# Kernel optimization log

Measured on AMD Instinct MI355X. Metric: run time of the kernel, lower is better.

## Reference

```python
import jax, jax.numpy as jnp
import numpy as np


def setup_inputs() -> dict:
    key = jax.random.key(0)
    ks = jax.random.split(key, 12)
    B, N, D_in, D = 64, 512, 512, 512
    inp = {
        "x": jax.random.normal(ks[0], (B, N, D_in), dtype=jnp.float32),
        "adj": jax.random.uniform(ks[1], (B, N, N), dtype=jnp.float32),
        "mask": jnp.ones((B, N, 1), dtype=jnp.float32),
        "W_enc": jax.random.normal(ks[2], (D_in, D), dtype=jnp.float32) * (1.0 / np.sqrt(D_in)),
        "b_enc": jnp.zeros((D,), dtype=jnp.float32),
        "Wz": jax.random.normal(ks[3], (D, D), dtype=jnp.float32) * (1.0 / np.sqrt(D)),
        "Uz": jax.random.normal(ks[4], (D, D), dtype=jnp.float32) * (1.0 / np.sqrt(D)),
        "bz": jnp.zeros((D,), dtype=jnp.float32),
        "Wr": jax.random.normal(ks[5], (D, D), dtype=jnp.float32) * (1.0 / np.sqrt(D)),
        "Ur": jax.random.normal(ks[6], (D, D), dtype=jnp.float32) * (1.0 / np.sqrt(D)),
        "br": jnp.zeros((D,), dtype=jnp.float32),
        "Wh": jax.random.normal(ks[7], (D, D), dtype=jnp.float32) * (1.0 / np.sqrt(D)),
        "Uh": jax.random.normal(ks[8], (D, D), dtype=jnp.float32) * (1.0 / np.sqrt(D)),
        "bh": jnp.zeros((D,), dtype=jnp.float32),
        "ba": jnp.zeros((D,), dtype=jnp.float32),
        "steps": 2,
    }
    return inp


def _gru_step(h, adj, mask, Wz, Uz, bz, Wr, Ur, br, Wh, Uh, bh, ba, act):
    # aggregated neighbor messages: [B,N,D]
    a = jnp.einsum('bnm,bmd->bnd', adj, h) + ba
    z = act(a @ Wz + h @ Uz + bz)          # update gate
    r = act(a @ Wr + h @ Ur + br)          # reset gate
    hc = jnp.tanh(a @ Wh + (r * h) @ Uh + bh)
    hc = hc * mask
    return (1.0 - z) * h + z * hc


def reference(x, adj, mask, W_enc, b_enc, Wz, Uz, bz, Wr, Ur, br, Wh, Uh, bh, ba, steps):
    act = jax.nn.relu
    h = mask * act(x @ W_enc + b_enc)      # [B,N,D]
    for _ in range(steps):
        h = _gru_step(h, adj, mask, Wz, Uz, bz, Wr, Ur, br, Wh, Uh, bh, ba, act)
    return h
```

## Files before the change

### kernel.cpp

```cpp
#include <hip/hip_runtime.h>


#define LD 512
#define CFENCE asm volatile("" ::: "memory")

typedef unsigned short u16;
typedef _Float16 f16;
typedef f16 f16x8 __attribute__((ext_vector_type(8)));
typedef float f32x4 __attribute__((ext_vector_type(4)));

__device__ __forceinline__ u16 f2h(float f) { f16 h = (f16)f; return *(u16*)&h; }
__device__ __forceinline__ float h2f(u16 b) { f16 h = *(f16*)&b; return (float)h; }

__device__ __forceinline__ void gload16(const void* g, void* l) {
  __builtin_amdgcn_global_load_lds(
      (const __attribute__((address_space(1))) void*)g,
      (__attribute__((address_space(3))) void*)l, 16, 0, 0);
}

__global__ void cvt_f16(const float* __restrict__ in, u16* __restrict__ out, int n4) {
  int i = blockIdx.x * blockDim.x + threadIdx.x;
  if (i >= n4) return;
  float4 v = reinterpret_cast<const float4*>(in)[i];
  ushort4 o;
  o.x = f2h(v.x); o.y = f2h(v.y); o.z = f2h(v.z); o.w = f2h(v.w);
  reinterpret_cast<ushort4*>(out)[i] = o;
}

__global__ void cvt2h(const float* __restrict__ in, u16* __restrict__ ohi,
                      u16* __restrict__ olo, int n4) {
  int i = blockIdx.x * blockDim.x + threadIdx.x;
  if (i >= n4) return;
  float4 v = reinterpret_cast<const float4*>(in)[i];
  ushort4 h, l;
  h.x = f2h(v.x); l.x = f2h(v.x - h2f(h.x));
  h.y = f2h(v.y); l.y = f2h(v.y - h2f(h.y));
  h.z = f2h(v.z); l.z = f2h(v.z - h2f(h.z));
  h.w = f2h(v.w); l.w = f2h(v.w - h2f(h.w));
  reinterpret_cast<ushort4*>(ohi)[i] = h;
  reinterpret_cast<ushort4*>(olo)[i] = l;
}

__global__ void wconv1(const float* __restrict__ in, u16* __restrict__ out, float scale) {
  __shared__ float sm[32][33];
  int tx = threadIdx.x & 31, ty = threadIdx.x >> 5;
  int k0 = blockIdx.y * 32, n0 = blockIdx.x * 32;
#pragma unroll
  for (int i = 0; i < 32; i += 8)
    sm[ty + i][tx] = in[(size_t)(k0 + ty + i) * LD + n0 + tx];
  __syncthreads();
#pragma unroll
  for (int i = 0; i < 32; i += 8)
    out[(size_t)(n0 + ty + i) * LD + k0 + tx] = f2h(sm[tx][ty + i] * scale);
}

__global__ void wconv2h(const float* __restrict__ in, u16* __restrict__ ohi,
                        u16* __restrict__ olo, float scale) {
  __shared__ float sm[32][33];
  int tx = threadIdx.x & 31, ty = threadIdx.x >> 5;
  int k0 = blockIdx.y * 32, n0 = blockIdx.x * 32;
#pragma unroll
  for (int i = 0; i < 32; i += 8)
    sm[ty + i][tx] = in[(size_t)(k0 + ty + i) * LD + n0 + tx];
  __syncthreads();
#pragma unroll
  for (int i = 0; i < 32; i += 8) {
    float v = sm[tx][ty + i] * scale;
    u16 hi = f2h(v);
    size_t o = (size_t)(n0 + ty + i) * LD + k0 + tx;
    ohi[o] = hi;
    olo[o] = f2h(v - h2f(hi));
  }
}

__global__ void transp16(const u16* __restrict__ in, u16* __restrict__ out) {
  __shared__ u16 sm[64][65];
  int b = blockIdx.z;
  int n0 = blockIdx.y * 64, d0 = blockIdx.x * 64;
  int lane = threadIdx.x & 63, grp = threadIdx.x >> 6;
  const u16* src = in + ((size_t)b * LD + n0) * LD + d0;
#pragma unroll
  for (int i = grp; i < 64; i += 4)
    sm[i][lane] = src[(size_t)i * LD + lane];
  __syncthreads();
  u16* dst = out + ((size_t)b * LD + d0) * LD + n0;
#pragma unroll
  for (int i = grp; i < 64; i += 4)
    dst[(size_t)i * LD + lane] = sm[lane][i];
}

struct Desc {
  const u16* A[6];
  const u16* B[6];
  long bsA, bsB;
  const float* bias1;
  const float* mask;
  const float* hf32;
  const u16* z16;
  float* outf;
  u16* o16;
  u16* o16b;
};

template <int MODE, int NA>
__global__ __launch_bounds__(512, 2) void gemm8(Desc d) {
  constexpr int NT = NA * 8;
  constexpr int GYB = (MODE == 1) ? 2 : 128;
  constexpr int RPB = (MODE == 1) ? 512 : 0;

  __shared__ __align__(16) u16 lds[65536];

  const int t = threadIdx.x;
  const int lane = t & 63;
  const int wid = t >> 6;
  const int wr = wid >> 2, wc = wid & 3;

  const int id = (int)blockIdx.x;
  const int swz = (id & 7) * 32 + (id >> 3);
  const int bx = swz & 1;
  const int by = (swz >> 1) % GYB;
  const size_t bz = (size_t)((swz >> 1) / GYB);

  const int lsw = lane & 7;
  const int lk = lane >> 4;
  const int rowA = wr * 128 + (lane & 15);
  const int rowB = wc * 64 + (lane & 15);
  int aofs[2], bofs[2];
#pragma unroll
  for (int ks = 0; ks < 2; ++ks) {
    aofs[ks] = rowA * 64 + (((ks * 4 + lk) ^ lsw) * 8);
    bofs[ks] = 16384 + rowB * 64 + (((ks * 4 + lk) ^ lsw) * 8);
  }

  f32x4 acc[8][4] = {};
  f16x8 bfr[8];

  const size_t rowOffA = (size_t)by * 256 * LD;
  const size_t rowOffB = (size_t)bx * 256 * LD;

  auto stagePair = [&](int tt, int ph) {
    const u16* Ap = d.A[tt >> 3] + bz * d.bsA + rowOffA;
    const u16* Bp = d.B[tt >> 3] + bz * d.bsB + rowOffB;
    const int kb = (tt & 7) * 64;
    u16* Lb = &lds[(tt & 1) * 32768];
    if (ph < 2) {
      const int i0 = t, i1 = t + 512;
      const int r0 = 128 * ph + (i0 >> 3), c0 = i0 & 7;
      const int r1 = 128 * ph + (i1 >> 3), c1 = i1 & 7;
      gload16(Bp + (size_t)r0 * LD + kb + ((c0 ^ (r0 & 7)) * 8),
              Lb + 16384 + r0 * 64 + c0 * 8);
      gload16(Bp + (size_t)r1 * LD + kb + ((c1 ^ (r1 & 7)) * 8),
              Lb + 16384 + r1 * 64 + c1 * 8);
    } else {
      const int s0 = 2 * (ph - 2), s1 = s0 + 1;
      const int rr = (t >> 8) * 128 + ((t >> 3) & 31), cc = t & 7;
      const int r0 = 32 * s0 + rr, r1 = 32 * s1 + rr;
      gload16(Ap + (size_t)r0 * LD + kb + ((cc ^ (r0 & 7)) * 8),
              Lb + r0 * 64 + cc * 8);
      gload16(Ap + (size_t)r1 * LD + kb + ((cc ^ (r1 & 7)) * 8),
              Lb + r1 * 64 + cc * 8);
    }
  };

  stagePair(0, 0); stagePair(0, 1); stagePair(0, 2); stagePair(0, 3);
  asm volatile("s_waitcnt vmcnt(2)" ::: "memory");
  __builtin_amdgcn_s_barrier();

  for (int tt = 0; tt < NT; ++tt) {
    const u16* L = &lds[(tt & 1) * 32768];
    const bool st = (tt + 1) < NT;
#pragma unroll
    for (int p = 0; p < 4; ++p) {
      if (p == 0) {
#pragma unroll
        for (int j = 0; j < 4; ++j)
#pragma unroll
          for (int ks = 0; ks < 2; ++ks)
            bfr[j * 2 + ks] = *(const f16x8*)&L[bofs[ks] + j * 1024];
      }
      f16x8 af[2][2];
#pragma unroll
      for (int di = 0; di < 2; ++di)
#pragma unroll
        for (int ks = 0; ks < 2; ++ks)
          af[di][ks] = *(const f16x8*)&L[aofs[ks] + (2 * p + di) * 1024];
      if (st) stagePair(tt + 1, p);
      __builtin_amdgcn_s_setprio(1);
#pragma unroll
      for (int di = 0; di < 2; ++di)
#pragma unroll
        for (int j = 0; j < 4; ++j) {
          acc[2 * p + di][j] = __builtin_amdgcn_mfma_f32_16x16x32_f16(
              af[di][0], bfr[j * 2 + 0], acc[2 * p + di][j], 0, 0, 0);
          acc[2 * p + di][j] = __builtin_amdgcn_mfma_f32_16x16x32_f16(
              af[di][1], bfr[j * 2 + 1], acc[2 * p + di][j], 0, 0, 0);
        }
      __builtin_amdgcn_s_setprio(0);
      if (p == 1) {
        if (st) asm volatile("s_waitcnt vmcnt(4)" ::: "memory");
        else    asm volatile("s_waitcnt vmcnt(0)" ::: "memory");
      } else if (p == 3) {
        if (st) asm volatile("s_waitcnt vmcnt(2)" ::: "memory");
      }
      CFENCE;
      __builtin_amdgcn_s_barrier();
    }
  }

  const float S4 = 0.0625f;
  const float S12 = 2.44140625e-4f;
  const int rowBase = (int)bz * RPB + by * 256 + wr * 128 + (lane >> 4) * 4;
  const int colBase = bx * 256 + wc * 64 + (lane & 15);
#pragma unroll
  for (int i = 0; i < 8; ++i) {
#pragma unroll
    for (int j = 0; j < 4; ++j) {
      const int col = colBase + j * 16;
      const float bv = d.bias1[col];
#pragma unroll
      for (int r = 0; r < 4; ++r) {
        const int row = rowBase + i * 16 + r;
        const size_t idx = (size_t)row * LD + col;
        const float a = acc[i][j][r];
        if (MODE == 0) {
          float v = fmaxf(a + bv, 0.0f) * d.mask[row];
          d.outf[idx] = v;
          d.o16[idx] = f2h(v * S4);
        } else if (MODE == 1) {
          float v = a + bv * S4;
          u16 hi = f2h(v);
          d.o16[idx] = hi;
          d.o16b[idx] = f2h(v - h2f(hi));
        } else if (MODE == 2) {
          float v = fmaxf(a + bv, 0.0f);
          d.o16[idx] = f2h(v * S4);
        } else if (MODE == 3) {
          float v = fmaxf(a + bv, 0.0f) * d.hf32[idx];
          u16 hi = f2h(v * S12);
          d.o16[idx] = hi;
          float rec = h2f(hi) * 4096.0f;
          d.o16b[idx] = f2h((v - rec) * S12);
        } else {
          float hc = tanhf(a + bv) * d.mask[row];
          float z = 16.0f * h2f(d.z16[idx]);
          float h = d.hf32[idx];
          float hn = (1.0f - z) * h + z * hc;
          d.outf[idx] = hn;
          d.o16[idx] = f2h(hn * S4);
        }
      }
    }
  }
}

extern "C" void kernel_launch(void* const* d_in, const int* in_sizes, int n_in,
                              void* d_out, int out_size, void* d_ws, size_t ws_size,
                              hipStream_t stream) {
  const float* x    = (const float*)d_in[0];
  const float* adj  = (const float*)d_in[1];
  const float* mask = (const float*)d_in[2];
  const float* Wenc = (const float*)d_in[3];
  const float* benc = (const float*)d_in[4];
  const float* Wz   = (const float*)d_in[5];
  const float* Uz   = (const float*)d_in[6];
  const float* bz_  = (const float*)d_in[7];
  const float* Wr   = (const float*)d_in[8];
  const float* Ur   = (const float*)d_in[9];
  const float* br_  = (const float*)d_in[10];
  const float* Wh   = (const float*)d_in[11];
  const float* Uh   = (const float*)d_in[12];
  const float* bh_  = (const float*)d_in[13];
  const float* ba_  = (const float*)d_in[14];

  float* hf = (float*)d_out;

  const size_t SZ  = (size_t)64 * 512 * 512 * sizeof(u16);
  const size_t WSZ = (size_t)LD * LD * sizeof(u16);
  const size_t NEED = 7 * SZ + 11 * WSZ;
  if (ws_size < NEED) return;

  char* p = (char*)d_ws;
  u16* adj16 = (u16*)p; p += SZ;
  u16* h16   = (u16*)p; p += SZ;
  u16* a_hi  = (u16*)p; p += SZ;
  u16* a_lo  = (u16*)p; p += SZ;
  u16* zht   = (u16*)p; p += SZ;
  u16* rh_hi = (u16*)p; p += SZ;
  u16* rh_lo = (u16*)p; p += SZ;
  u16* w     = (u16*)p;
  u16* We_h = w + 0 * LD * LD;  u16* We_l = w + 1 * LD * LD;
  u16* Wz1  = w + 2 * LD * LD;
  u16* Uz1  = w + 3 * LD * LD;
  u16* Wr_h = w + 4 * LD * LD;  u16* Wr_l = w + 5 * LD * LD;
  u16* Ur1  = w + 6 * LD * LD;
  u16* Wh_h = w + 7 * LD * LD;  u16* Wh_l = w + 8 * LD * LD;
  u16* Uh_h = w + 9 * LD * LD;  u16* Uh_l = w + 10 * LD * LD;
  u16* x_hi = a_hi;
  u16* x_lo = a_lo;

  const int NELT = 64 * 512 * 512;
  cvt2h<<<NELT / 4 / 256, 256, 0, stream>>>(x, x_hi, x_lo, NELT / 4);
  cvt_f16<<<NELT / 4 / 256, 256, 0, stream>>>(adj, adj16, NELT / 4);

  dim3 wg(16, 16);
  wconv2h<<<wg, 256, 0, stream>>>(Wenc, We_h, We_l, 1.0f);
  wconv1<<<wg, 256, 0, stream>>>(Wz, Wz1, 16.0f);
  wconv1<<<wg, 256, 0, stream>>>(Uz, Uz1, 16.0f);
  wconv2h<<<wg, 256, 0, stream>>>(Wr, Wr_h, Wr_l, 16.0f);
  wconv1<<<wg, 256, 0, stream>>>(Ur, Ur1, 16.0f);
  wconv2h<<<wg, 256, 0, stream>>>(Wh, Wh_h, Wh_l, 16.0f);
  wconv2h<<<wg, 256, 0, stream>>>(Uh, Uh_h, Uh_l, 4096.0f);

  const long NN = (long)LD * LD;

  {
    Desc d{};
    d.A[0] = x_hi; d.B[0] = We_h;
    d.A[1] = x_lo; d.B[1] = We_h;
    d.A[2] = x_hi; d.B[2] = We_l;
    d.bias1 = benc; d.mask = mask; d.outf = hf; d.o16 = h16;
    gemm8<0, 3><<<256, 512, 0, stream>>>(d);
  }

  for (int s = 0; s < 2; ++s) {
    transp16<<<dim3(8, 8, 64), 256, 0, stream>>>(h16, zht);
    {
      Desc d{};
      d.A[0] = adj16; d.B[0] = zht; d.bsA = NN; d.bsB = NN;
      d.bias1 = ba_; d.o16 = a_hi; d.o16b = a_lo;
      gemm8<1, 1><<<256, 512, 0, stream>>>(d);
    }
    {
      Desc d{};
      d.A[0] = a_hi; d.B[0] = Wz1;
      d.A[1] = h16;  d.B[1] = Uz1;
      d.bias1 = bz_; d.o16 = zht;
      gemm8<2, 2><<<256, 512, 0, stream>>>(d);
    }
    {
      Desc d{};
      d.A[0] = a_hi; d.B[0] = Wr_h;
      d.A[1] = a_hi; d.B[1] = Wr_l;
      d.A[2] = a_lo; d.B[2] = Wr_h;
      d.A[3] = h16;  d.B[3] = Ur1;
      d.bias1 = br_; d.hf32 = hf; d.o16 = rh_hi; d.o16b = rh_lo;
      gemm8<3, 4><<<256, 512, 0, stream>>>(d);
    }
    if (s == 0) {
      Desc d{};
      d.A[0] = a_hi;  d.B[0] = Wh_h;
      d.A[1] = a_hi;  d.B[1] = Wh_l;
      d.A[2] = a_lo;  d.B[2] = Wh_h;
      d.A[3] = rh_hi; d.B[3] = Uh_h;
      d.A[4] = rh_hi; d.B[4] = Uh_l;
      d.A[5] = rh_lo; d.B[5] = Uh_h;
      d.bias1 = bh_; d.mask = mask; d.hf32 = hf; d.z16 = zht;
      d.outf = hf; d.o16 = h16;
      gemm8<4, 6><<<256, 512, 0, stream>>>(d);
    } else {
      Desc d{};
      d.A[0] = a_hi;  d.B[0] = Wh_h;
      d.A[1] = rh_hi; d.B[1] = Uh_h;
      d.bias1 = bh_; d.mask = mask; d.hf32 = hf; d.z16 = zht;
      d.outf = hf; d.o16 = h16;
      gemm8<4, 2><<<256, 512, 0, stream>>>(d);
    }
  }
}
```

Before: 736.2 us.

## Halve GEMM tile rows, triple-buffer LDS, and split GRU work into batch-half chunks

The GEMM kernel shrinks its output tile from 256x256 to 128x256 and uses three LDS buffers, prefetching two k-tiles ahead instead of one. Each phase is now launched as two 256-block chunks over half the rows or batches, so the per-launch grid stays the same with half the work per block. Chunking per batch half may also keep intermediates such as a_hi/a_lo and zht in cache between dependent kernels. In exchange it doubles the number of launches, lowers arithmetic intensity per block, and adds barriers per k-step.

```diff
diff --git a/kernel.cpp b/kernel.cpp
--- a/kernel.cpp
+++ b/kernel.cpp
@@ -93,6 +93,8 @@
   const u16* A[6];
   const u16* B[6];
   long bsA, bsB;
+  int rowOff;
+  int bzOff;
   const float* bias1;
   const float* mask;
   const float* hf32;
@@ -102,13 +104,13 @@
   u16* o16b;
 };
 
+#define BUFU 24576
+
 template <int MODE, int NA>
-__global__ __launch_bounds__(512, 2) void gemm8(Desc d) {
+__global__ __launch_bounds__(512, 2) void gemm9(Desc d) {
   constexpr int NT = NA * 8;
-  constexpr int GYB = (MODE == 1) ? 2 : 128;
-  constexpr int RPB = (MODE == 1) ? 512 : 0;
-
-  __shared__ __align__(16) u16 lds[65536];
+
+  __shared__ __align__(16) u16 lds[3 * BUFU];
 
   const int t = threadIdx.x;
   const int lane = t & 63;
@@ -118,101 +120,147 @@
   const int id = (int)blockIdx.x;
   const int swz = (id & 7) * 32 + (id >> 3);
   const int bx = swz & 1;
-  const int by = (swz >> 1) % GYB;
-  const size_t bz = (size_t)((swz >> 1) / GYB);
+  size_t baseA, baseB;
+  int rowBase0;
+  if (MODE == 1) {
+    const int by2 = (swz >> 1) & 3;
+    const size_t bz = (size_t)(swz >> 3) + d.bzOff;
+    baseA = bz * d.bsA + (size_t)by2 * 128 * LD;
+    baseB = bz * d.bsB + (size_t)bx * 256 * LD;
+    rowBase0 = (int)bz * 512 + by2 * 128;
+  } else {
+    const int by = swz >> 1;
+    baseA = (size_t)(d.rowOff + by * 128) * LD;
+    baseB = (size_t)bx * 256 * LD;
+    rowBase0 = d.rowOff + by * 128;
+  }
+
+  const int sr = t >> 3;
+  const int sc = ((t & 7) ^ (sr & 7)) * 8;
 
   const int lsw = lane & 7;
   const int lk = lane >> 4;
-  const int rowA = wr * 128 + (lane & 15);
+  const int rowA = wr * 64 + (lane & 15);
   const int rowB = wc * 64 + (lane & 15);
   int aofs[2], bofs[2];
 #pragma unroll
   for (int ks = 0; ks < 2; ++ks) {
     aofs[ks] = rowA * 64 + (((ks * 4 + lk) ^ lsw) * 8);
-    bofs[ks] = 16384 + rowB * 64 + (((ks * 4 + lk) ^ lsw) * 8);
-  }
-
-  f32x4 acc[8][4] = {};
-  f16x8 bfr[8];
-
-  const size_t rowOffA = (size_t)by * 256 * LD;
-  const size_t rowOffB = (size_t)bx * 256 * LD;
-
-  auto stagePair = [&](int tt, int ph) {
-    const u16* Ap = d.A[tt >> 3] + bz * d.bsA + rowOffA;
-    const u16* Bp = d.B[tt >> 3] + bz * d.bsB + rowOffB;
-    const int kb = (tt & 7) * 64;
-    u16* Lb = &lds[(tt & 1) * 32768];
-    if (ph < 2) {
-      const int i0 = t, i1 = t + 512;
-      const int r0 = 128 * ph + (i0 >> 3), c0 = i0 & 7;
-      const int r1 = 128 * ph + (i1 >> 3), c1 = i1 & 7;
-      gload16(Bp + (size_t)r0 * LD + kb + ((c0 ^ (r0 & 7)) * 8),
-              Lb + 16384 + r0 * 64 + c0 * 8);
-      gload16(Bp + (size_t)r1 * LD + kb + ((c1 ^ (r1 & 7)) * 8),
-              Lb + 16384 + r1 * 64 + c1 * 8);
+    bofs[ks] = 8192 + rowB * 64 + (((ks * 4 + lk) ^ lsw) * 8);
+  }
+
+  f32x4 acc[4][4] = {};
+
+  auto stage3 = [&](const u16* ApS, const u16* BpS, int kbS, u16* LS, int ph) {
+    if (ph == 0) {
+#pragma unroll
+      for (int k = 0; k < 3; ++k)
+        gload16(BpS + (size_t)(sr + 64 * k) * LD + kbS + sc,
+                LS + 8192 + (t + 512 * k) * 8);
     } else {
-      const int s0 = 2 * (ph - 2), s1 = s0 + 1;
-      const int rr = (t >> 8) * 128 + ((t >> 3) & 31), cc = t & 7;
-      const int r0 = 32 * s0 + rr, r1 = 32 * s1 + rr;
-      gload16(Ap + (size_t)r0 * LD + kb + ((cc ^ (r0 & 7)) * 8),
-              Lb + r0 * 64 + cc * 8);
-      gload16(Ap + (size_t)r1 * LD + kb + ((cc ^ (r1 & 7)) * 8),
-              Lb + r1 * 64 + cc * 8);
+      gload16(BpS + (size_t)(sr + 192) * LD + kbS + sc, LS + 8192 + (t + 1536) * 8);
+#pragma unroll
+      for (int k = 0; k < 2; ++k)
+        gload16(ApS + (size_t)(sr + 64 * k) * LD + kbS + sc, LS + (t + 512 * k) * 8);
     }
   };
 
-  stagePair(0, 0); stagePair(0, 1); stagePair(0, 2); stagePair(0, 3);
-  asm volatile("s_waitcnt vmcnt(2)" ::: "memory");
+  {
+    const u16* Ap0 = d.A[0] + baseA;
+    const u16* Bp0 = d.B[0] + baseB;
+    stage3(Ap0, Bp0, 0, lds, 0);
+    stage3(Ap0, Bp0, 0, lds, 1);
+    stage3(Ap0, Bp0, 64, lds + BUFU, 0);
+    stage3(Ap0, Bp0, 64, lds + BUFU, 1);
+  }
+  asm volatile("s_waitcnt vmcnt(6)" ::: "memory");
   __builtin_amdgcn_s_barrier();
 
-  for (int tt = 0; tt < NT; ++tt) {
-    const u16* L = &lds[(tt & 1) * 32768];
-    const bool st = (tt + 1) < NT;
-#pragma unroll
-    for (int p = 0; p < 4; ++p) {
-      if (p == 0) {
-#pragma unroll
-        for (int j = 0; j < 4; ++j)
-#pragma unroll
-          for (int ks = 0; ks < 2; ++ks)
-            bfr[j * 2 + ks] = *(const f16x8*)&L[bofs[ks] + j * 1024];
-      }
-      f16x8 af[2][2];
+  int bR = 0;
+#pragma unroll
+  for (int s = 0; s < NA; ++s) {
+    const u16* Ap = d.A[s] + baseA;
+    const u16* Bp = d.B[s] + baseB;
+    const u16* ApN = d.A[s + 1 < NA ? s + 1 : s] + baseA;
+    const u16* BpN = d.B[s + 1 < NA ? s + 1 : s] + baseB;
+    for (int kt = 0; kt < 8; ++kt) {
+      const int tt = s * 8 + kt;
+      const u16* L = lds + bR * BUFU;
+      u16* LS = lds + (bR >= 1 ? bR - 1 : 2) * BUFU;
+      const bool st = (tt + 2) < NT;
+      const u16* ApS = kt < 6 ? Ap : ApN;
+      const u16* BpS = kt < 6 ? Bp : BpN;
+      const int kbS = ((kt + 2) & 7) * 64;
+
+      f16x8 bfr[4][2], af0[2][2];
+#pragma unroll
+      for (int j = 0; j < 4; ++j)
+#pragma unroll
+        for (int ks = 0; ks < 2; ++ks)
+          bfr[j][ks] = *(const f16x8*)&L[bofs[ks] + j * 1024];
 #pragma unroll
       for (int di = 0; di < 2; ++di)
 #pragma unroll
         for (int ks = 0; ks < 2; ++ks)
-          af[di][ks] = *(const f16x8*)&L[aofs[ks] + (2 * p + di) * 1024];
-      if (st) stagePair(tt + 1, p);
+          af0[di][ks] = *(const f16x8*)&L[aofs[ks] + di * 1024];
+      if (st) stage3(ApS, BpS, kbS, LS, 0);
+      CFENCE;
+      __builtin_amdgcn_s_barrier();
+      asm volatile("s_waitcnt lgkmcnt(0)" ::: "memory");
+      __builtin_amdgcn_sched_barrier(0);
       __builtin_amdgcn_s_setprio(1);
 #pragma unroll
       for (int di = 0; di < 2; ++di)
 #pragma unroll
         for (int j = 0; j < 4; ++j) {
-          acc[2 * p + di][j] = __builtin_amdgcn_mfma_f32_16x16x32_f16(
-              af[di][0], bfr[j * 2 + 0], acc[2 * p + di][j], 0, 0, 0);
-          acc[2 * p + di][j] = __builtin_amdgcn_mfma_f32_16x16x32_f16(
-              af[di][1], bfr[j * 2 + 1], acc[2 * p + di][j], 0, 0, 0);
+          acc[di][j] = __builtin_amdgcn_mfma_f32_16x16x32_f16(
+              af0[di][0], bfr[j][0], acc[di][j], 0, 0, 0);
+          acc[di][j] = __builtin_amdgcn_mfma_f32_16x16x32_f16(
+              af0[di][1], bfr[j][1], acc[di][j], 0, 0, 0);
         }
       __builtin_amdgcn_s_setprio(0);
-      if (p == 1) {
-        if (st) asm volatile("s_waitcnt vmcnt(4)" ::: "memory");
-        else    asm volatile("s_waitcnt vmcnt(0)" ::: "memory");
-      } else if (p == 3) {
-        if (st) asm volatile("s_waitcnt vmcnt(2)" ::: "memory");
-      }
       CFENCE;
       __builtin_amdgcn_s_barrier();
+
+      f16x8 af1[2][2];
+#pragma unroll
+      for (int di = 0; di < 2; ++di)
+#pragma unroll
+        for (int ks = 0; ks < 2; ++ks)
+          af1[di][ks] = *(const f16x8*)&L[aofs[ks] + (2 + di) * 1024];
+      if (st) stage3(ApS, BpS, kbS, LS, 1);
+      CFENCE;
+      __builtin_amdgcn_s_barrier();
+      asm volatile("s_waitcnt lgkmcnt(0)" ::: "memory");
+      __builtin_amdgcn_sched_barrier(0);
+      __builtin_amdgcn_s_setprio(1);
+#pragma unroll
+      for (int di = 0; di < 2; ++di)
+#pragma unroll
+        for (int j = 0; j < 4; ++j) {
+          acc[2 + di][j] = __builtin_amdgcn_mfma_f32_16x16x32_f16(
+              af1[di][0], bfr[j][0], acc[2 + di][j], 0, 0, 0);
+          acc[2 + di][j] = __builtin_amdgcn_mfma_f32_16x16x32_f16(
+              af1[di][1], bfr[j][1], acc[2 + di][j], 0, 0, 0);
+        }
+      __builtin_amdgcn_s_setprio(0);
+      if (st) {
+        asm volatile("s_waitcnt vmcnt(6)" ::: "memory");
+      } else {
+        asm volatile("s_waitcnt vmcnt(0)" ::: "memory");
+      }
+      CFENCE;
+      __builtin_amdgcn_s_barrier();
+      bR = bR == 2 ? 0 : bR + 1;
     }
   }
 
   const float S4 = 0.0625f;
   const float S12 = 2.44140625e-4f;
-  const int rowBase = (int)bz * RPB + by * 256 + wr * 128 + (lane >> 4) * 4;
+  const int rowBase = rowBase0 + wr * 64 + (lane >> 4) * 4;
   const int colBase = bx * 256 + wc * 64 + (lane & 15);
 #pragma unroll
-  for (int i = 0; i < 8; ++i) {
+  for (int i = 0; i < 4; ++i) {
 #pragma unroll
     for (int j = 0; j < 4; ++j) {
       const int col = colBase + j * 16;
@@ -313,57 +361,65 @@
 
   const long NN = (long)LD * LD;
 
-  {
+  for (int ch = 0; ch < 2; ++ch) {
     Desc d{};
     d.A[0] = x_hi; d.B[0] = We_h;
     d.A[1] = x_lo; d.B[1] = We_h;
     d.A[2] = x_hi; d.B[2] = We_l;
+    d.rowOff = ch * 16384;
     d.bias1 = benc; d.mask = mask; d.outf = hf; d.o16 = h16;
-    gemm8<0, 3><<<256, 512, 0, stream>>>(d);
+    gemm9<0, 3><<<256, 512, 0, stream>>>(d);
   }
 
   for (int s = 0; s < 2; ++s) {
     transp16<<<dim3(8, 8, 64), 256, 0, stream>>>(h16, zht);
-    {
-      Desc d{};
-      d.A[0] = adj16; d.B[0] = zht; d.bsA = NN; d.bsB = NN;
-      d.bias1 = ba_; d.o16 = a_hi; d.o16b = a_lo;
-      gemm8<1, 1><<<256, 512, 0, stream>>>(d);
+    for (int ch = 0; ch < 2; ++ch) {
+      {
+        Desc d{};
+        d.A[0] = adj16; d.B[0] = zht; d.bsA = NN; d.bsB = NN;
+        d.bzOff = ch * 32;
+        d.bias1 = ba_; d.o16 = a_hi; d.o16b = a_lo;
+        gemm9<1, 1><<<256, 512, 0, stream>>>(d);
+      }
+      {
+        Desc d{};
+        d.A[0] = a_hi; d.B[0] = Wz1;
+        d.A[1] = h16;  d.B[1] = Uz1;
+        d.rowOff = ch * 16384;
+        d.bias1 = bz_; d.o16 = zht;
+        gemm9<2, 2><<<256, 512, 0, stream>>>(d);
+      }
+      {
+        Desc d{};
+        d.A[0] = a_hi; d.B[0] = Wr_h;
+        d.A[1] = a_hi; d.B[1] = Wr_l;
+        d.A[2] = a_lo; d.B[2] = Wr_h;
+        d.A[3] = h16;  d.B[3] = Ur1;
+        d.rowOff = ch * 16384;
+        d.bias1 = br_; d.hf32 = hf; d.o16 = rh_hi; d.o16b = rh_lo;
+        gemm9<3, 4><<<256, 512, 0, stream>>>(d);
+      }
+      if (s == 0) {
+        Desc d{};
+        d.A[0] = a_hi;  d.B[0] = Wh_h;
+        d.A[1] = a_hi;  d.B[1] = Wh_l;
+        d.A[2] = a_lo;  d.B[2] = Wh_h;
+        d.A[3] = rh_hi; d.B[3] = Uh_h;
+        d.A[4] = rh_hi; d.B[4] = Uh_l;
+        d.A[5] = rh_lo; d.B[5] = Uh_h;
+        d.rowOff = ch * 16384;
+        d.bias1 = bh_; d.mask = mask; d.hf32 = hf; d.z16 = zht;
+        d.outf = hf; d.o16 = h16;
+        gemm9<4, 6><<<256, 512, 0, stream>>>(d);
+      } else {
+        Desc d{};
+        d.A[0] = a_hi;  d.B[0] = Wh_h;
+        d.A[1] = rh_hi; d.B[1] = Uh_h;
+        d.rowOff = ch * 16384;
+        d.bias1 = bh_; d.mask = mask; d.hf32 = hf; d.z16 = zht;
+        d.outf = hf; d.o16 = h16;
+        gemm9<4, 2><<<256, 512, 0, stream>>>(d);
+      }
     }
-    {
-      Desc d{};
-      d.A[0] = a_hi; d.B[0] = Wz1;
-      d.A[1] = h16;  d.B[1] = Uz1;
-      d.bias1 = bz_; d.o16 = zht;
-      gemm8<2, 2><<<256, 512, 0, stream>>>(d);
-    }
-    {
-      Desc d{};
-      d.A[0] = a_hi; d.B[0] = Wr_h;
-      d.A[1] = a_hi; d.B[1] = Wr_l;
-      d.A[2] = a_lo; d.B[2] = Wr_h;
-      d.A[3] = h16;  d.B[3] = Ur1;
-      d.bias1 = br_; d.hf32 = hf; d.o16 = rh_hi; d.o16b = rh_lo;
-      gemm8<3, 4><<<256, 512, 0, stream>>>(d);
-    }
-    if (s == 0) {
-      Desc d{};
-      d.A[0] = a_hi;  d.B[0] = Wh_h;
-      d.A[1] = a_hi;  d.B[1] = Wh_l;
-      d.A[2] = a_lo;  d.B[2] = Wh_h;
-      d.A[3] = rh_hi; d.B[3] = Uh_h;
-      d.A[4] = rh_hi; d.B[4] = Uh_l;
-      d.A[5] = rh_lo; d.B[5] = Uh_h;
-      d.bias1 = bh_; d.mask = mask; d.hf32 = hf; d.z16 = zht;
-      d.outf = hf; d.o16 = h16;
-      gemm8<4, 6><<<256, 512, 0, stream>>>(d);
-    } else {
-      Desc d{};
-      d.A[0] = a_hi;  d.B[0] = Wh_h;
-      d.A[1] = rh_hi; d.B[1] = Uh_h;
-      d.bias1 = bh_; d.mask = mask; d.hf32 = hf; d.z16 = zht;
-      d.outf = hf; d.o16 = h16;
-      gemm8<4, 2><<<256, 512, 0, stream>>>(d);
-    }
-  }
-}
+  }
+}
```

After: 771.4 us. 4.8% more time.
